# Performance work log

Measured on AMD Instinct MI355X. Metric: run time of the kernel, lower is better.

## Reference

```python
import jax, jax.numpy as jnp
import numpy as np

B, N, C = 4, 2048, 256
H = 8
DH = C // H
WIN = 16
SCALE = DH ** -0.5


def setup_inputs() -> dict:
    key = jax.random.key(0)
    k1, k2, k3, k4 = jax.random.split(key, 4)
    x = jax.random.normal(k1, (B, N, C), dtype=jnp.float32)
    # qkv: nn.Linear(dim, 3*dim, bias=False); store as [C, 3C] for x @ W
    W_qkv = jax.random.normal(k2, (C, 3 * C), dtype=jnp.float32) * (C ** -0.5)
    # proj: nn.Linear(dim, dim) with bias
    W_proj = jax.random.normal(k3, (C, C), dtype=jnp.float32) * (C ** -0.5)
    b_proj = jax.random.normal(k4, (C,), dtype=jnp.float32) * 0.01
    return {"x": x, "W_qkv": W_qkv, "W_proj": W_proj, "b_proj": b_proj}


def reference(x, W_qkv, W_proj, b_proj):
    Bs, Ns, Cs = x.shape
    # qkv projection -> q, k, v each [B, H, N, Dh]
    qkv = (x @ W_qkv).reshape(Bs, Ns, 3, H, DH).transpose(2, 0, 3, 1, 4)
    q, k, v = qkv[0], qkv[1], qkv[2]

    # --- global dense attention ---
    attn_global = jax.nn.softmax(jnp.einsum('bhnd,bhmd->bhnm', q, k) * SCALE, axis=-1)
    x_global = jnp.einsum('bhnm,bhmd->bhnd', attn_global, v)  # [B,H,N,Dh]

    # --- non-overlapping local window attention (vectorized over windows) ---
    nw = Ns // WIN
    qw = q.reshape(Bs, H, nw, WIN, DH)
    kw = k.reshape(Bs, H, nw, WIN, DH)
    vw = v.reshape(Bs, H, nw, WIN, DH)
    attn_local = jax.nn.softmax(jnp.einsum('bhwid,bhwjd->bhwij', qw, kw) * SCALE, axis=-1)
    x_local = jnp.einsum('bhwij,bhwjd->bhwid', attn_local, vw).reshape(Bs, H, Ns, DH)

    # combine, merge heads, output projection
    x_out = (x_global + x_local).transpose(0, 2, 1, 3).reshape(Bs, Ns, Cs)
    x_out = x_out @ W_proj + b_proj
    weights = jax.lax.stop_gradient(attn_global)
    return (x_out, weights)
```

## Files before the change

### kernel.cpp

```cpp
#include <hip/hip_runtime.h>
#include <hip/hip_bf16.h>

#define B_ 4
#define N_ 2048
#define C_ 256
#define H_ 8
#define DH_ 32
#define SCALE_ 0.17677669529663687f

typedef __attribute__((ext_vector_type(8))) short bf16x8;
typedef __attribute__((ext_vector_type(4))) float f32x4;

__device__ __forceinline__ short f2bf(float f) {
    union { float f; unsigned u; } v; v.f = f;
    unsigned r = v.u + 0x7fffu + ((v.u >> 16) & 1u);
    return (short)(r >> 16);
}
__device__ __forceinline__ float bf2f(short s) {
    union { unsigned u; float f; } v; v.u = ((unsigned)(unsigned short)s) << 16;
    return v.f;
}

__global__ __launch_bounds__(256) void k_qkv(
    const float* __restrict__ x, const float* __restrict__ Wq,
    short* __restrict__ qbf, short* __restrict__ kbf, short* __restrict__ vtbf)
{
    __shared__ __align__(16) short XSh[64*40], XSl[64*40];
    __shared__ __align__(16) short WTh[128*40], WTl[128*40];
    const int tid = threadIdx.x;
    const int wid = tid >> 6, lane = tid & 63;
    const int l15 = lane & 15, quad = lane >> 4;
    const int r0 = blockIdx.y * 64;
    const int c0 = blockIdx.x * 128;

    f32x4 acc[8];
    #pragma unroll
    for (int t = 0; t < 8; ++t) acc[t] = (f32x4){0.f,0.f,0.f,0.f};

    for (int kk = 0; kk < 8; ++kk) {
        const int k0 = kk * 32;
        {
            int row = tid >> 2, cg = tid & 3;
            const float* xp = &x[(size_t)(r0 + row) * C_ + k0 + cg * 8];
            float4 a = *(const float4*)xp;
            float4 b = *(const float4*)(xp + 4);
            float vals[8] = {a.x,a.y,a.z,a.w,b.x,b.y,b.z,b.w};
            short hi[8], lo[8];
            #pragma unroll
            for (int i = 0; i < 8; ++i) {
                hi[i] = f2bf(vals[i]);
                lo[i] = f2bf(vals[i] - bf2f(hi[i]));
            }
            *(bf16x8*)&XSh[row*40 + cg*8] = *(bf16x8*)hi;
            *(bf16x8*)&XSl[row*40 + cg*8] = *(bf16x8*)lo;
        }
        {
            int wrow = tid >> 3, seg = tid & 7;
            const float* wp = &Wq[(size_t)(k0 + wrow) * (3*C_) + c0 + seg*16];
            #pragma unroll
            for (int q4 = 0; q4 < 4; ++q4) {
                float4 wv = *(const float4*)(wp + q4*4);
                float wa[4] = {wv.x, wv.y, wv.z, wv.w};
                #pragma unroll
                for (int i = 0; i < 4; ++i) {
                    int col = seg*16 + q4*4 + i;
                    short hb = f2bf(wa[i]);
                    WTh[col*40 + wrow] = hb;
                    WTl[col*40 + wrow] = f2bf(wa[i] - bf2f(hb));
                }
            }
        }
        __syncthreads();
        bf16x8 ah = *(bf16x8*)&XSh[(wid*16 + l15)*40 + quad*8];
        bf16x8 al = *(bf16x8*)&XSl[(wid*16 + l15)*40 + quad*8];
        #pragma unroll
        for (int t = 0; t < 8; ++t) {
            bf16x8 bh = *(bf16x8*)&WTh[(t*16 + l15)*40 + quad*8];
            bf16x8 bl = *(bf16x8*)&WTl[(t*16 + l15)*40 + quad*8];
            acc[t] = __builtin_amdgcn_mfma_f32_16x16x32_bf16(ah, bh, acc[t], 0,0,0);
            acc[t] = __builtin_amdgcn_mfma_f32_16x16x32_bf16(ah, bl, acc[t], 0,0,0);
            acc[t] = __builtin_amdgcn_mfma_f32_16x16x32_bf16(al, bh, acc[t], 0,0,0);
        }
        __syncthreads();
    }
    #pragma unroll
    for (int t = 0; t < 8; ++t) {
        int j = c0 + t*16 + l15;
        int which = j >> 8, h = (j >> 5) & 7, d = j & 31;
        #pragma unroll
        for (int r = 0; r < 4; ++r) {
            int tok = r0 + wid*16 + quad*4 + r;
            int b = tok >> 11, n = tok & (N_-1);
            float val = acc[t][r];
            int bh = b * H_ + h;
            if (which == 0)      qbf[((size_t)bh * N_ + n) * DH_ + d] = f2bf(val * SCALE_);
            else if (which == 1) kbf[((size_t)bh * N_ + n) * DH_ + d] = f2bf(val);
            else                 vtbf[((size_t)bh * DH_ + d) * N_ + n] = f2bf(val);
        }
    }
}

__global__ __launch_bounds__(256) void k_zsum(
    const short* __restrict__ qbf, const short* __restrict__ kbf,
    float* __restrict__ zrecip)
{
    const int tid = threadIdx.x;
    const int wid = tid >> 6, lane = tid & 63;
    const int l15 = lane & 15, quad = lane >> 4;
    const int bh = blockIdx.y;
    const int q0 = blockIdx.x * 64 + wid * 16;

    bf16x8 aq = *(const bf16x8*)&qbf[((size_t)bh * N_ + q0 + l15) * DH_ + quad * 8];
    float zs[4] = {0.f, 0.f, 0.f, 0.f};
    const short* kbase = &kbf[(size_t)bh * N_ * DH_];
    #pragma unroll 4
    for (int mt = 0; mt < N_/16; ++mt) {
        bf16x8 bk = *(const bf16x8*)&kbase[(mt*16 + l15) * DH_ + quad * 8];
        f32x4 S = __builtin_amdgcn_mfma_f32_16x16x32_bf16(aq, bk, (f32x4){0,0,0,0}, 0,0,0);
        zs[0] += __expf(S[0]); zs[1] += __expf(S[1]);
        zs[2] += __expf(S[2]); zs[3] += __expf(S[3]);
    }
    #pragma unroll
    for (int r = 0; r < 4; ++r)
        for (int off = 1; off < 16; off <<= 1)
            zs[r] += __shfl_xor(zs[r], off, 64);
    if (l15 == 0) {
        #pragma unroll
        for (int r = 0; r < 4; ++r)
            zrecip[(size_t)bh * N_ + q0 + quad*4 + r] = 1.0f / zs[r];
    }
}

__global__ __launch_bounds__(256) void k_attn(
    const short* __restrict__ qbf, const short* __restrict__ kbf,
    const short* __restrict__ vtbf, const float* __restrict__ zrecip,
    float* __restrict__ wout, short* __restrict__ xc)
{
    __shared__ __align__(16) short pt[4][16*40];
    const int tid = threadIdx.x;
    const int wid = tid >> 6, lane = tid & 63;
    const int l15 = lane & 15, quad = lane >> 4;
    const int bh = blockIdx.y;
    const int b = bh >> 3, h = bh & 7;
    const int q0 = blockIdx.x * 64 + wid * 16;
    const int w = q0 >> 4;
    const int mtd = w >> 1, hl = w & 1;

    bf16x8 aq = *(const bf16x8*)&qbf[((size_t)bh * N_ + q0 + l15) * DH_ + quad * 8];
    float zr[4];
    #pragma unroll
    for (int r = 0; r < 4; ++r) zr[r] = zrecip[(size_t)bh * N_ + q0 + quad*4 + r];

    const short* kbase = &kbf[(size_t)bh * N_ * DH_];
    const short* vbase = &vtbf[(size_t)bh * DH_ * N_];
    float* wbase = &wout[((size_t)bh * N_ + q0) * N_];

    f32x4 O0 = {0,0,0,0}, O1 = {0,0,0,0};
    float pl[4] = {0.f,0.f,0.f,0.f};
    short* myp = pt[wid];

    for (int mt = 0; mt < N_/32; ++mt) {
        const int m0 = mt * 32;
        bf16x8 bk0 = *(const bf16x8*)&kbase[(size_t)(m0 + l15) * DH_ + quad * 8];
        bf16x8 bk1 = *(const bf16x8*)&kbase[(size_t)(m0 + 16 + l15) * DH_ + quad * 8];
        f32x4 S0 = __builtin_amdgcn_mfma_f32_16x16x32_bf16(aq, bk0, (f32x4){0,0,0,0}, 0,0,0);
        f32x4 S1 = __builtin_amdgcn_mfma_f32_16x16x32_bf16(aq, bk1, (f32x4){0,0,0,0}, 0,0,0);
        float p0[4], p1[4];
        #pragma unroll
        for (int r = 0; r < 4; ++r) { p0[r] = __expf(S0[r]); p1[r] = __expf(S1[r]); }
        if (mt == mtd) {
            #pragma unroll
            for (int r = 0; r < 4; ++r) pl[r] = hl ? p1[r] : p0[r];
        }
        #pragma unroll
        for (int r = 0; r < 4; ++r) {
            float wp0 = p0[r] * zr[r];
            float wp1 = p1[r] * zr[r];
            float* wrow = wbase + (size_t)(quad*4 + r) * N_ + m0;
            wrow[l15]      = wp0;
            wrow[16 + l15] = wp1;
            myp[(quad*4 + r)*40 + l15]      = f2bf(wp0);
            myp[(quad*4 + r)*40 + 16 + l15] = f2bf(wp1);
        }
        bf16x8 ap  = *(bf16x8*)&myp[l15*40 + quad*8];
        bf16x8 bv0 = *(const bf16x8*)&vbase[(size_t)l15 * N_ + m0 + quad*8];
        bf16x8 bv1 = *(const bf16x8*)&vbase[(size_t)(16 + l15) * N_ + m0 + quad*8];
        O0 = __builtin_amdgcn_mfma_f32_16x16x32_bf16(ap, bv0, O0, 0,0,0);
        O1 = __builtin_amdgcn_mfma_f32_16x16x32_bf16(ap, bv1, O1, 0,0,0);
    }

    float zl[4];
    #pragma unroll
    for (int r = 0; r < 4; ++r) {
        zl[r] = pl[r];
        for (int off = 1; off < 16; off <<= 1)
            zl[r] += __shfl_xor(zl[r], off, 64);
    }
    #pragma unroll
    for (int r = 0; r < 4; ++r) {
        float pn = pl[r] / zl[r];
        myp[(quad*4 + r)*40 + l15]      = hl ? (short)0 : f2bf(pn);
        myp[(quad*4 + r)*40 + 16 + l15] = hl ? f2bf(pn) : (short)0;
    }
    {
        const int m0 = mtd * 32;
        bf16x8 ap  = *(bf16x8*)&myp[l15*40 + quad*8];
        bf16x8 bv0 = *(const bf16x8*)&vbase[(size_t)l15 * N_ + m0 + quad*8];
        bf16x8 bv1 = *(const bf16x8*)&vbase[(size_t)(16 + l15) * N_ + m0 + quad*8];
        O0 = __builtin_amdgcn_mfma_f32_16x16x32_bf16(ap, bv0, O0, 0,0,0);
        O1 = __builtin_amdgcn_mfma_f32_16x16x32_bf16(ap, bv1, O1, 0,0,0);
    }
    #pragma unroll
    for (int r = 0; r < 4; ++r) {
        int n = q0 + quad*4 + r;
        short* xrow = &xc[((size_t)(b * N_ + n)) * C_ + h * DH_];
        xrow[l15]      = f2bf(O0[r]);
        xrow[16 + l15] = f2bf(O1[r]);
    }
}

__global__ __launch_bounds__(256) void k_proj(
    const short* __restrict__ xc, const float* __restrict__ Wp,
    const float* __restrict__ bp, float* __restrict__ out)
{
    __shared__ __align__(16) short WT[64 * 264];
    const int tid = threadIdx.x;
    const int wid = tid >> 6, lane = tid & 63;
    const int l15 = lane & 15, quad = lane >> 4;
    const int c0 = blockIdx.x * 64;
    const int r0 = blockIdx.y * 64;

    {
        int k = tid;
        const float* wp = &Wp[(size_t)k * C_ + c0];
        #pragma unroll
        for (int s = 0; s < 16; ++s) {
            float4 wv = *(const float4*)(wp + s*4);
            float wa[4] = {wv.x, wv.y, wv.z, wv.w};
            #pragma unroll
            for (int i = 0; i < 4; ++i)
                WT[(s*4 + i) * 264 + k] = f2bf(wa[i]);
        }
    }
    __syncthreads();

    f32x4 acc[4];
    #pragma unroll
    for (int t = 0; t < 4; ++t) acc[t] = (f32x4){0,0,0,0};
    const short* xrow = &xc[(size_t)(r0 + wid*16 + l15) * C_];
    #pragma unroll
    for (int kk = 0; kk < 8; ++kk) {
        bf16x8 a = *(const bf16x8*)&xrow[kk*32 + quad*8];
        #pragma unroll
        for (int t = 0; t < 4; ++t) {
            bf16x8 bw = *(bf16x8*)&WT[(t*16 + l15) * 264 + kk*32 + quad*8];
            acc[t] = __builtin_amdgcn_mfma_f32_16x16x32_bf16(a, bw, acc[t], 0,0,0);
        }
    }
    #pragma unroll
    for (int t = 0; t < 4; ++t) {
        int j = c0 + t*16 + l15;
        float bias = bp[j];
        #pragma unroll
        for (int r = 0; r < 4; ++r) {
            int row = r0 + wid*16 + quad*4 + r;
            out[(size_t)row * C_ + j] = acc[t][r] + bias;
        }
    }
}

extern "C" void kernel_launch(void* const* d_in, const int* in_sizes, int n_in,
                              void* d_out, int out_size, void* d_ws, size_t ws_size,
                              hipStream_t stream)
{
    const float* x  = (const float*)d_in[0];
    const float* Wq = (const float*)d_in[1];
    const float* Wp = (const float*)d_in[2];
    const float* bp = (const float*)d_in[3];
    float* out  = (float*)d_out;
    float* wout = out + (size_t)B_ * N_ * C_;

    char* ws = (char*)d_ws;
    short* qbf  = (short*)ws;
    short* kbf  = qbf  + (size_t)B_*H_*N_*DH_;
    short* vtbf = kbf  + (size_t)B_*H_*N_*DH_;
    float* zrecip = (float*)(vtbf + (size_t)B_*H_*N_*DH_);
    short* xc   = (short*)(zrecip + (size_t)B_*H_*N_);

    k_qkv <<<dim3(6, 128),  256, 0, stream>>>(x, Wq, qbf, kbf, vtbf);
    k_zsum<<<dim3(32, 32),  256, 0, stream>>>(qbf, kbf, zrecip);
    k_attn<<<dim3(32, 32),  256, 0, stream>>>(qbf, kbf, vtbf, zrecip, wout, xc);
    k_proj<<<dim3(4, 128),  256, 0, stream>>>(xc, Wp, bp, out);
}
```

Baseline: 703.8 us.

## Stage fp32 attention probs in LDS to emit vectorized nontemporal weight stores

The attention kernel now writes fp32 probabilities into a padded LDS tile, then reads them back transposed so each lane holds 8 contiguous columns of one row. This lets the 2048x2048 weight output be written with 16-byte nontemporal vector stores instead of scattered scalar stores, and the bf16 MFMA operand is built with packed hardware conversions. It doubles LDS traffic per tile, and the conversion now uses the v_cvt_pk_bf16_f32 inline asm in place of the software rounding.

```diff
diff --git a/kernel.cpp b/kernel.cpp
--- a/kernel.cpp
+++ b/kernel.cpp
@@ -19,6 +19,14 @@
 __device__ __forceinline__ float bf2f(short s) {
     union { unsigned u; float f; } v; v.u = ((unsigned)(unsigned short)s) << 16;
     return v.f;
+}
+__device__ __forceinline__ bf16x8 cvt_pk8(f32x4 a, f32x4 b) {
+    union { unsigned u[4]; bf16x8 v; } r;
+    asm("v_cvt_pk_bf16_f32 %0, %1, %2" : "=v"(r.u[0]) : "v"(a[0]), "v"(a[1]));
+    asm("v_cvt_pk_bf16_f32 %0, %1, %2" : "=v"(r.u[1]) : "v"(a[2]), "v"(a[3]));
+    asm("v_cvt_pk_bf16_f32 %0, %1, %2" : "=v"(r.u[2]) : "v"(b[0]), "v"(b[1]));
+    asm("v_cvt_pk_bf16_f32 %0, %1, %2" : "=v"(r.u[3]) : "v"(b[2]), "v"(b[3]));
+    return r.v;
 }
 
 __global__ __launch_bounds__(256) void k_qkv(
@@ -136,7 +144,7 @@
     const short* __restrict__ vtbf, const float* __restrict__ zrecip,
     float* __restrict__ wout, short* __restrict__ xc)
 {
-    __shared__ __align__(16) short pt[4][16*40];
+    __shared__ __align__(16) float pt[4][16*36];
     const int tid = threadIdx.x;
     const int wid = tid >> 6, lane = tid & 63;
     const int l15 = lane & 15, quad = lane >> 4;
@@ -157,7 +165,10 @@
 
     f32x4 O0 = {0,0,0,0}, O1 = {0,0,0,0};
     float pl[4] = {0.f,0.f,0.f,0.f};
-    short* myp = pt[wid];
+    float* myp = pt[wid];
+    float*       wr0  = &myp[(quad*4)*36 + l15];
+    const float* rd   = &myp[l15*36 + quad*8];
+    float*       wrow = wbase + (size_t)l15 * N_ + quad*8;
 
     for (int mt = 0; mt < N_/32; ++mt) {
         const int m0 = mt * 32;
@@ -174,15 +185,14 @@
         }
         #pragma unroll
         for (int r = 0; r < 4; ++r) {
-            float wp0 = p0[r] * zr[r];
-            float wp1 = p1[r] * zr[r];
-            float* wrow = wbase + (size_t)(quad*4 + r) * N_ + m0;
-            wrow[l15]      = wp0;
-            wrow[16 + l15] = wp1;
-            myp[(quad*4 + r)*40 + l15]      = f2bf(wp0);
-            myp[(quad*4 + r)*40 + 16 + l15] = f2bf(wp1);
-        }
-        bf16x8 ap  = *(bf16x8*)&myp[l15*40 + quad*8];
+            wr0[r*36]      = p0[r] * zr[r];
+            wr0[r*36 + 16] = p1[r] * zr[r];
+        }
+        f32x4 pa0 = *(const f32x4*)rd;
+        f32x4 pa1 = *(const f32x4*)(rd + 4);
+        __builtin_nontemporal_store(pa0, (f32x4*)(wrow + m0));
+        __builtin_nontemporal_store(pa1, (f32x4*)(wrow + m0 + 4));
+        bf16x8 ap = cvt_pk8(pa0, pa1);
         bf16x8 bv0 = *(const bf16x8*)&vbase[(size_t)l15 * N_ + m0 + quad*8];
         bf16x8 bv1 = *(const bf16x8*)&vbase[(size_t)(16 + l15) * N_ + m0 + quad*8];
         O0 = __builtin_amdgcn_mfma_f32_16x16x32_bf16(ap, bv0, O0, 0,0,0);
@@ -199,12 +209,14 @@
     #pragma unroll
     for (int r = 0; r < 4; ++r) {
         float pn = pl[r] / zl[r];
-        myp[(quad*4 + r)*40 + l15]      = hl ? (short)0 : f2bf(pn);
-        myp[(quad*4 + r)*40 + 16 + l15] = hl ? f2bf(pn) : (short)0;
+        wr0[r*36]      = hl ? 0.f : pn;
+        wr0[r*36 + 16] = hl ? pn : 0.f;
     }
     {
         const int m0 = mtd * 32;
-        bf16x8 ap  = *(bf16x8*)&myp[l15*40 + quad*8];
+        f32x4 pa0 = *(const f32x4*)rd;
+        f32x4 pa1 = *(const f32x4*)(rd + 4);
+        bf16x8 ap = cvt_pk8(pa0, pa1);
         bf16x8 bv0 = *(const bf16x8*)&vbase[(size_t)l15 * N_ + m0 + quad*8];
         bf16x8 bv1 = *(const bf16x8*)&vbase[(size_t)(16 + l15) * N_ + m0 + quad*8];
         O0 = __builtin_amdgcn_mfma_f32_16x16x32_bf16(ap, bv0, O0, 0,0,0);
```

After: 732.0 us. +4.0%, slower.
